# Optimization experiments

Hardware: AMD Instinct MI355X
Metric: run time of the kernel (lower is better)

The kernel has to match this reference:

```python
import jax, jax.numpy as jnp
import numpy as np

HID = 1024
NTOK = 16
BIAS_SCALE = 1.5
EPS = 1e-5


def layer_norm(x, g, b):
    mu = jnp.mean(x, axis=-1, keepdims=True)
    var = jnp.mean(jnp.square(x - mu), axis=-1, keepdims=True)
    return (x - mu) * jax.lax.rsqrt(var + EPS) * g + b


def setup_inputs() -> dict:
    key = jax.random.key(0)
    ks = jax.random.split(key, 16)
    B, T = 8, 4096
    Dt, Ds, Dp = 512, 512, 64
    Din = Dt + Ds + Dp

    def lin(k, fan_in, fan_out):
        bound = 1.0 / np.sqrt(fan_in)
        k1, k2 = jax.random.split(k)
        W = jax.random.uniform(k1, (fan_in, fan_out), jnp.float32, -bound, bound)
        b = jax.random.uniform(k2, (fan_out,), jnp.float32, -bound, bound)
        return W, b

    W_in, b_in = lin(ks[0], Din, HID)
    W_m1, b_m1 = lin(ks[1], HID, HID)
    W_m2, b_m2 = lin(ks[2], HID, HID)
    W_o1, b_o1 = lin(ks[3], HID, HID // 2)
    W_o2, b_o2 = lin(ks[4], HID // 2, 1)
    return {
        "trace_features": jax.random.normal(ks[5], (B, T, Dt), jnp.float32),
        "semantic_features": jax.random.normal(ks[6], (B, T, Ds), jnp.float32),
        "prior_features": jax.random.normal(ks[7], (B, T, Dp), jnp.float32),
        "W_in": W_in, "b_in": b_in,
        "ln_in_g": jnp.ones((HID,), jnp.float32), "ln_in_b": jnp.zeros((HID,), jnp.float32),
        "W_m1": W_m1, "b_m1": b_m1, "W_m2": W_m2, "b_m2": b_m2,
        "W_o1": W_o1, "b_o1": b_o1, "W_o2": W_o2, "b_o2": b_o2,
        "token_queries": jax.random.normal(ks[8], (NTOK, HID), jnp.float32) * 0.02,
        "ln_out_g": jnp.ones((HID,), jnp.float32), "ln_out_b": jnp.zeros((HID,), jnp.float32),
    }


def reference(trace_features, semantic_features, prior_features,
              W_in, b_in, ln_in_g, ln_in_b,
              W_m1, b_m1, W_m2, b_m2,
              W_o1, b_o1, W_o2, b_o2,
              token_queries, ln_out_g, ln_out_b):
    # fuse inputs: [B, T, Dt+Ds+Dp]
    fused = jnp.concatenate([trace_features, semantic_features, prior_features], axis=-1)
    h = fused @ W_in + b_in  # [B, T, H]
    mlp = jax.nn.gelu(h @ W_m1 + b_m1, approximate=False) @ W_m2 + b_m2
    seq_hidden = layer_norm(h + mlp, ln_in_g, ln_in_b)

    # objectness head -> [B, T]
    obj_logits = (jax.nn.gelu(seq_hidden @ W_o1 + b_o1, approximate=False) @ W_o2 + b_o2)[..., 0]
    objectness = jax.nn.sigmoid(obj_logits)

    # learned-query cross attention with objectness bias
    scale = float(HID) ** -0.5
    attn_logits = jnp.einsum('nh,bth->bnt', token_queries, seq_hidden) * scale
    attn_logits = attn_logits + BIAS_SCALE * objectness[:, None, :]
    attn = jax.nn.softmax(attn_logits, axis=-1)  # [B, N, T]
    token_values = jnp.einsum('bnt,bth->bnh', attn, seq_hidden)
    state_tokens = layer_norm(token_queries[None] + token_values, ln_out_g, ln_out_b)
    return state_tokens, attn, objectness
```

## Files before the change

### kernel.cpp

```cpp
#include <hip/hip_runtime.h>
#include <hip/hip_bf16.h>
#include <math.h>

typedef __bf16 bf16;
typedef __bf16 bf16x8 __attribute__((ext_vector_type(8)));
typedef __bf16 bf16x4 __attribute__((ext_vector_type(4)));
typedef float f32x4 __attribute__((ext_vector_type(4)));

#define KM 32768

__device__ __forceinline__ void gload16(const void* g, void* l) {
  __builtin_amdgcn_global_load_lds((const __attribute__((address_space(1))) void*)g,
                                   (__attribute__((address_space(3))) void*)l, 16, 0, 0);
}

__device__ __forceinline__ float gelu_exact(float x) {
  return 0.5f * x * (1.0f + erff(x * 0.70710678118654752f));
}

__global__ void fuse_kernel(const float* __restrict__ tr, const float* __restrict__ se,
                            const float* __restrict__ pr, bf16* __restrict__ Xb) {
  int g = blockIdx.x * 256 + threadIdx.x;
  if (g >= KM * 272) return;
  int m = g / 272;
  int k0 = (g - m * 272) * 4;
  float4 v;
  if (k0 < 512)       v = *reinterpret_cast<const float4*>(tr + (size_t)m * 512 + k0);
  else if (k0 < 1024) v = *reinterpret_cast<const float4*>(se + (size_t)m * 512 + (k0 - 512));
  else                v = *reinterpret_cast<const float4*>(pr + (size_t)m * 64 + (k0 - 1024));
  union { bf16 h[4]; ushort4 u; } p;
  p.h[0] = (bf16)v.x; p.h[1] = (bf16)v.y; p.h[2] = (bf16)v.z; p.h[3] = (bf16)v.w;
  *reinterpret_cast<ushort4*>(Xb + (size_t)m * 1088 + k0) = p.u;
}

__global__ void transpose_all(const float* __restrict__ W_in, const float* __restrict__ W_m1,
                              const float* __restrict__ W_m2, const float* __restrict__ W_o1,
                              bf16* __restrict__ WbIn, bf16* __restrict__ WbM1,
                              bf16* __restrict__ WbM2, bf16* __restrict__ WbO1) {
  __shared__ float t[32][33];
  int b = blockIdx.x;
  const float* W; bf16* Wt; int K, N, kb, nb;
  if (b < 1088)      { W = W_in; Wt = WbIn; K = 1088; N = 1024; kb = b % 34;  nb = b / 34; }
  else if (b < 2112) { int c = b - 1088; W = W_m1; Wt = WbM1; K = 1024; N = 1024; kb = c & 31; nb = c >> 5; }
  else if (b < 3136) { int c = b - 2112; W = W_m2; Wt = WbM2; K = 1024; N = 1024; kb = c & 31; nb = c >> 5; }
  else               { int c = b - 3136; W = W_o1; Wt = WbO1; K = 1024; N = 512;  kb = c & 31; nb = c >> 5; }
  int k0 = kb * 32, n0 = nb * 32;
  int tx = threadIdx.x & 31, ty = threadIdx.x >> 5;
  #pragma unroll
  for (int j = 0; j < 32; j += 8) t[ty + j][tx] = W[(size_t)(k0 + ty + j) * N + n0 + tx];
  __syncthreads();
  #pragma unroll
  for (int j = 0; j < 32; j += 8)
    Wt[(size_t)(n0 + ty + j) * K + k0 + tx] = (bf16)t[tx][ty + j];
}

template<int ACT, bool RES, bool OBJ>
__global__ void gemm_kernel(const bf16* __restrict__ A, const bf16* __restrict__ Bt,
                            const float* __restrict__ bias, const bf16* __restrict__ res,
                            bf16* __restrict__ C, const float* __restrict__ w2,
                            float* __restrict__ objp, int N, int K, int nbn) {
  __shared__ __align__(16) bf16 lds[2][128 * 64];
  int nwg = gridDim.x;
  int bid0 = blockIdx.x;
  int bid = (nwg & 7) ? bid0 : ((bid0 & 7) * (nwg >> 3) + (bid0 >> 3));
  int bn = bid % nbn, bm = bid / nbn;
  int tid = threadIdx.x;
  int w = tid >> 6, L = tid & 63;
  int wm = w >> 1, wn = w & 1;
  int srow = L >> 3;
  int scol = 8 * ((L & 7) ^ srow);
  const bf16* Ab = A + (size_t)(bm * 128) * K;
  const bf16* Bb = Bt + (size_t)(bn * 128) * K;
  f32x4 acc[4][4] = {};
  int nkt = (K + 63) >> 6;
  for (int kt = 0; kt < nkt; ++kt) {
    int k0 = kt << 6;
    #pragma unroll
    for (int i = 0; i < 4; ++i) {
      int row = w * 32 + i * 8;
      gload16(Ab + (size_t)(row + srow) * K + k0 + scol, &lds[0][row * 64]);
      gload16(Bb + (size_t)(row + srow) * K + k0 + scol, &lds[1][row * 64]);
    }
    __syncthreads();
    #pragma unroll
    for (int kk = 0; kk < 2; ++kk) {
      bf16x8 af[4], bfr[4];
      int cb = kk * 64 + ((L >> 4) * 16);
      #pragma unroll
      for (int m = 0; m < 4; ++m) {
        int r = wm * 64 + m * 16 + (L & 15);
        int addr = r * 128 + (cb ^ ((r & 7) << 4));
        af[m] = *reinterpret_cast<const bf16x8*>(
            reinterpret_cast<const char*>(&lds[0][0]) + addr);
      }
      #pragma unroll
      for (int n = 0; n < 4; ++n) {
        int r = wn * 64 + n * 16 + (L & 15);
        int addr = r * 128 + (cb ^ ((r & 7) << 4));
        bfr[n] = *reinterpret_cast<const bf16x8*>(
            reinterpret_cast<const char*>(&lds[1][0]) + addr);
      }
      #pragma unroll
      for (int m = 0; m < 4; ++m)
        #pragma unroll
        for (int n = 0; n < 4; ++n)
          acc[m][n] = __builtin_amdgcn_mfma_f32_16x16x32_bf16(af[m], bfr[n], acc[m][n], 0, 0, 0);
    }
    __syncthreads();
  }
  int cn0 = bn * 128 + wn * 64;
  float bv[4];
  #pragma unroll
  for (int n = 0; n < 4; ++n) bv[n] = bias[cn0 + n * 16 + (L & 15)];
  if (OBJ) {
    float w2v[4];
    #pragma unroll
    for (int n = 0; n < 4; ++n) w2v[n] = w2[cn0 + n * 16 + (L & 15)];
    float* op = objp + (size_t)(bn * 2 + wn) * KM;
    #pragma unroll
    for (int m = 0; m < 4; ++m) {
      int grow0 = bm * 128 + wm * 64 + m * 16 + ((L >> 4) << 2);
      #pragma unroll
      for (int r = 0; r < 4; ++r) {
        float s = 0.f;
        #pragma unroll
        for (int n = 0; n < 4; ++n) {
          float v = gelu_exact(acc[m][n][r] + bv[n]);
          s += v * w2v[n];
        }
        s += __shfl_xor(s, 1); s += __shfl_xor(s, 2);
        s += __shfl_xor(s, 4); s += __shfl_xor(s, 8);
        if ((L & 15) == 0) op[grow0 + r] = s;
      }
    }
  } else {
    #pragma unroll
    for (int m = 0; m < 4; ++m) {
      int grow0 = bm * 128 + wm * 64 + m * 16 + ((L >> 4) << 2);
      #pragma unroll
      for (int r = 0; r < 4; ++r) {
        size_t ro = (size_t)(grow0 + r) * N;
        #pragma unroll
        for (int n = 0; n < 4; ++n) {
          float v = acc[m][n][r] + bv[n];
          if (ACT == 1) v = gelu_exact(v);
          int col = cn0 + n * 16 + (L & 15);
          if (RES) v += (float)res[ro + col];
          C[ro + col] = (bf16)v;
        }
      }
    }
  }
}

__global__ void ln_wave_kernel(bf16* __restrict__ X, const float* __restrict__ g,
                               const float* __restrict__ b) {
  int w = threadIdx.x >> 6, L = threadIdx.x & 63;
  size_t row = (size_t)blockIdx.x * 4 + w;
  bf16* xr = X + row * 1024 + L * 16;
  bf16x8 v0 = *reinterpret_cast<const bf16x8*>(xr);
  bf16x8 v1 = *reinterpret_cast<const bf16x8*>(xr + 8);
  float x[16];
  #pragma unroll
  for (int i = 0; i < 8; ++i) { x[i] = (float)v0[i]; x[8 + i] = (float)v1[i]; }
  float s = 0.f;
  #pragma unroll
  for (int i = 0; i < 16; ++i) s += x[i];
  #pragma unroll
  for (int off = 32; off > 0; off >>= 1) s += __shfl_xor(s, off);
  float mu = s * (1.0f / 1024.0f);
  float sq = 0.f;
  #pragma unroll
  for (int i = 0; i < 16; ++i) { x[i] -= mu; sq += x[i] * x[i]; }
  #pragma unroll
  for (int off = 32; off > 0; off >>= 1) sq += __shfl_xor(sq, off);
  float rs = rsqrtf(sq * (1.0f / 1024.0f) + 1e-5f);
  const float4* gp = reinterpret_cast<const float4*>(g + L * 16);
  const float4* bp = reinterpret_cast<const float4*>(b + L * 16);
  bf16x8 o0, o1;
  #pragma unroll
  for (int q = 0; q < 4; ++q) {
    float4 gv = gp[q], bv = bp[q];
    int i = q * 4;
    float r0 = x[i] * rs * gv.x + bv.x;
    float r1 = x[i + 1] * rs * gv.y + bv.y;
    float r2 = x[i + 2] * rs * gv.z + bv.z;
    float r3 = x[i + 3] * rs * gv.w + bv.w;
    if (q < 2) { o0[i] = (bf16)r0; o0[i + 1] = (bf16)r1; o0[i + 2] = (bf16)r2; o0[i + 3] = (bf16)r3; }
    else { o1[i - 8] = (bf16)r0; o1[i - 7] = (bf16)r1; o1[i - 6] = (bf16)r2; o1[i - 5] = (bf16)r3; }
  }
  *reinterpret_cast<bf16x8*>(xr) = o0;
  *reinterpret_cast<bf16x8*>(xr + 8) = o1;
}

__global__ void attn_logits_mfma(const bf16* __restrict__ seq, const float* __restrict__ tq,
                                 const float* __restrict__ objp, const float* __restrict__ b2,
                                 float* __restrict__ logits, float* __restrict__ out_obj) {
  __shared__ bf16 tqs[16][1032];
  int tid = threadIdx.x;
  for (int i = tid; i < 4096; i += 256) {
    int idx = i * 4;
    int n = idx >> 10, k = idx & 1023;
    float4 v = *reinterpret_cast<const float4*>(tq + idx);
    bf16x4 p; p[0] = (bf16)v.x; p[1] = (bf16)v.y; p[2] = (bf16)v.z; p[3] = (bf16)v.w;
    *reinterpret_cast<bf16x4*>(&tqs[n][k]) = p;
  }
  __syncthreads();
  int w = tid >> 6, L = tid & 63;
  int row0 = blockIdx.x * 128 + w * 32;
  const bf16* A0 = seq + (size_t)(row0 + (L & 15)) * 1024 + ((L >> 4) * 8);
  const bf16* Bq = &tqs[L & 15][(L >> 4) * 8];
  f32x4 acc0 = {}, acc1 = {};
  #pragma unroll 4
  for (int kt = 0; kt < 32; ++kt) {
    int k0 = kt * 32;
    bf16x8 bq = *reinterpret_cast<const bf16x8*>(Bq + k0);
    bf16x8 a0 = *reinterpret_cast<const bf16x8*>(A0 + k0);
    bf16x8 a1 = *reinterpret_cast<const bf16x8*>(A0 + 16 * 1024 + k0);
    acc0 = __builtin_amdgcn_mfma_f32_16x16x32_bf16(a0, bq, acc0, 0, 0, 0);
    acc1 = __builtin_amdgcn_mfma_f32_16x16x32_bf16(a1, bq, acc1, 0, 0, 0);
  }
  float b2v = b2[0];
  int b = row0 >> 12;
  int n = L & 15;
  float* outn = logits + ((size_t)(b * 16) + n) * 4096;
  #pragma unroll
  for (int mf = 0; mf < 2; ++mf) {
    int mrow = row0 + mf * 16 + ((L >> 4) << 2);
    float os0 = 0.f, os1 = 0.f, os2 = 0.f, os3 = 0.f;
    #pragma unroll
    for (int p = 0; p < 8; ++p) {
      float4 t = *reinterpret_cast<const float4*>(objp + (size_t)p * KM + mrow);
      os0 += t.x; os1 += t.y; os2 += t.z; os3 += t.w;
    }
    float ob[4];
    ob[0] = 1.0f / (1.0f + expf(-(os0 + b2v)));
    ob[1] = 1.0f / (1.0f + expf(-(os1 + b2v)));
    ob[2] = 1.0f / (1.0f + expf(-(os2 + b2v)));
    ob[3] = 1.0f / (1.0f + expf(-(os3 + b2v)));
    #pragma unroll
    for (int r = 0; r < 4; ++r) {
      int m = mrow + r;
      float v = (mf == 0 ? acc0[r] : acc1[r]) * 0.03125f + 1.5f * ob[r];
      outn[m & 4095] = v;
    }
    if (n == 0) {
      float4 o4 = make_float4(ob[0], ob[1], ob[2], ob[3]);
      *reinterpret_cast<float4*>(out_obj + mrow) = o4;
    }
  }
}

__global__ void softmax_kernel(const float* __restrict__ logits, float* __restrict__ attn) {
  __shared__ float sb[4];
  size_t row = blockIdx.x;
  const float* lr = logits + row * 4096;
  float* orow = attn + row * 4096;
  int tid = threadIdx.x;
  float x[16];
  #pragma unroll
  for (int i = 0; i < 4; ++i) {
    float4 v = *reinterpret_cast<const float4*>(lr + tid * 16 + i * 4);
    x[i * 4 + 0] = v.x; x[i * 4 + 1] = v.y; x[i * 4 + 2] = v.z; x[i * 4 + 3] = v.w;
  }
  float mx = -1e30f;
  #pragma unroll
  for (int j = 0; j < 16; ++j) mx = fmaxf(mx, x[j]);
  #pragma unroll
  for (int off = 32; off > 0; off >>= 1) mx = fmaxf(mx, __shfl_xor(mx, off));
  if ((tid & 63) == 0) sb[tid >> 6] = mx;
  __syncthreads();
  mx = fmaxf(fmaxf(sb[0], sb[1]), fmaxf(sb[2], sb[3]));
  __syncthreads();
  float s = 0.f;
  #pragma unroll
  for (int j = 0; j < 16; ++j) { x[j] = expf(x[j] - mx); s += x[j]; }
  #pragma unroll
  for (int off = 32; off > 0; off >>= 1) s += __shfl_xor(s, off);
  if ((tid & 63) == 0) sb[tid >> 6] = s;
  __syncthreads();
  float inv = 1.0f / (sb[0] + sb[1] + sb[2] + sb[3]);
  #pragma unroll
  for (int i = 0; i < 4; ++i) {
    float4 v = make_float4(x[i * 4] * inv, x[i * 4 + 1] * inv, x[i * 4 + 2] * inv, x[i * 4 + 3] * inv);
    *reinterpret_cast<float4*>(orow + tid * 16 + i * 4) = v;
  }
}

__global__ void token_values_kernel(const float* __restrict__ attn, const bf16* __restrict__ seq,
                                    float* __restrict__ tvp) {
  int bid = blockIdx.x;
  int split = bid & 3;
  int hc = (bid >> 2) & 15;
  int b = bid >> 6;
  __shared__ float al[16][256];
  int h = hc * 64 + (threadIdx.x & 63);
  int grp = threadIdx.x >> 6;
  float acc[4] = {0.f, 0.f, 0.f, 0.f};
  for (int c = 0; c < 4; ++c) {
    int t0 = split * 1024 + c * 256;
    __syncthreads();
    for (int i = threadIdx.x; i < 4096; i += 256)
      al[i >> 8][i & 255] = attn[((size_t)b * 16 + (i >> 8)) * 4096 + t0 + (i & 255)];
    __syncthreads();
    for (int tt = 0; tt < 256; ++tt) {
      float s = (float)seq[((size_t)b * 4096 + t0 + tt) * 1024 + h];
      #pragma unroll
      for (int i = 0; i < 4; ++i) acc[i] += al[grp * 4 + i][tt] * s;
    }
  }
  #pragma unroll
  for (int i = 0; i < 4; ++i)
    tvp[(size_t)split * 131072 + ((size_t)b * 16 + grp * 4 + i) * 1024 + h] = acc[i];
}

__global__ void final_ln_kernel(const float* __restrict__ tq, const float* __restrict__ tvp,
                                const float* __restrict__ g, const float* __restrict__ bb,
                                float* __restrict__ out0) {
  __shared__ float sb[4];
  int row = blockIdx.x;
  int n = row & 15;
  int tid = threadIdx.x;
  float x[4];
  #pragma unroll
  for (int i = 0; i < 4; ++i) {
    int h = tid * 4 + i;
    float v = tq[n * 1024 + h];
    #pragma unroll
    for (int p = 0; p < 4; ++p) v += tvp[(size_t)p * 131072 + (size_t)row * 1024 + h];
    x[i] = v;
  }
  float s = x[0] + x[1] + x[2] + x[3];
  #pragma unroll
  for (int off = 32; off > 0; off >>= 1) s += __shfl_xor(s, off);
  if ((tid & 63) == 0) sb[tid >> 6] = s;
  __syncthreads();
  float mu = (sb[0] + sb[1] + sb[2] + sb[3]) * (1.0f / 1024.0f);
  __syncthreads();
  float d[4], sq = 0.f;
  #pragma unroll
  for (int i = 0; i < 4; ++i) { d[i] = x[i] - mu; sq += d[i] * d[i]; }
  #pragma unroll
  for (int off = 32; off > 0; off >>= 1) sq += __shfl_xor(sq, off);
  if ((tid & 63) == 0) sb[tid >> 6] = sq;
  __syncthreads();
  float var = (sb[0] + sb[1] + sb[2] + sb[3]) * (1.0f / 1024.0f);
  float rs = rsqrtf(var + 1e-5f);
  #pragma unroll
  for (int i = 0; i < 4; ++i) {
    int h = tid * 4 + i;
    out0[(size_t)row * 1024 + h] = d[i] * rs * g[h] + bb[h];
  }
}

extern "C" void kernel_launch(void* const* d_in, const int* in_sizes, int n_in,
                              void* d_out, int out_size, void* d_ws, size_t ws_size,
                              hipStream_t stream) {
  const float* tr      = (const float*)d_in[0];
  const float* se      = (const float*)d_in[1];
  const float* pr      = (const float*)d_in[2];
  const float* W_in    = (const float*)d_in[3];
  const float* b_in    = (const float*)d_in[4];
  const float* ln_in_g = (const float*)d_in[5];
  const float* ln_in_b = (const float*)d_in[6];
  const float* W_m1    = (const float*)d_in[7];
  const float* b_m1    = (const float*)d_in[8];
  const float* W_m2    = (const float*)d_in[9];
  const float* b_m2    = (const float*)d_in[10];
  const float* W_o1    = (const float*)d_in[11];
  const float* b_o1    = (const float*)d_in[12];
  const float* W_o2    = (const float*)d_in[13];
  const float* b_o2    = (const float*)d_in[14];
  const float* tq      = (const float*)d_in[15];
  const float* ln_out_g= (const float*)d_in[16];
  const float* ln_out_b= (const float*)d_in[17];

  float* out       = (float*)d_out;
  float* out_state = out;
  float* out_attn  = out + 131072;
  float* out_obj   = out + 131072 + 524288;

  char* ws = (char*)d_ws;
  size_t off = 0;
  auto alloc = [&](size_t bytes) {
    char* p = ws + off;
    off += (bytes + 255) & ~(size_t)255;
    return p;
  };
  bf16*  Xb   = (bf16*)alloc(71303168);
  bf16*  t1   = Xb;
  bf16*  hb   = (bf16*)alloc(67108864);
  bf16*  sq   = (bf16*)alloc(67108864);
  bf16*  WbIn = (bf16*)alloc(2228224);
  bf16*  WbM1 = (bf16*)alloc(2097152);
  bf16*  WbM2 = (bf16*)alloc(2097152);
  bf16*  WbO1 = (bf16*)alloc(1048576);
  float* objp = (float*)alloc(8 * KM * 4);
  float* logw = (float*)alloc(2097152);
  float* tvp  = (float*)alloc(2097152);

  fuse_kernel<<<(KM * 272 + 255) / 256, 256, 0, stream>>>(tr, se, pr, Xb);
  transpose_all<<<3648, 256, 0, stream>>>(W_in, W_m1, W_m2, W_o1, WbIn, WbM1, WbM2, WbO1);

  gemm_kernel<0, false, false><<<2048, 256, 0, stream>>>(
      Xb, WbIn, b_in, nullptr, hb, nullptr, nullptr, 1024, 1088, 8);
  gemm_kernel<1, false, false><<<2048, 256, 0, stream>>>(
      hb, WbM1, b_m1, nullptr, t1, nullptr, nullptr, 1024, 1024, 8);
  gemm_kernel<0, true, false><<<2048, 256, 0, stream>>>(
      t1, WbM2, b_m2, hb, sq, nullptr, nullptr, 1024, 1024, 8);
  ln_wave_kernel<<<8192, 256, 0, stream>>>(sq, ln_in_g, ln_in_b);
  gemm_kernel<1, false, true><<<1024, 256, 0, stream>>>(
      sq, WbO1, b_o1, nullptr, nullptr, W_o2, objp, 512, 1024, 4);
  attn_logits_mfma<<<256, 256, 0, stream>>>(sq, tq, objp, b_o2, logw, out_obj);
  softmax_kernel<<<128, 256, 0, stream>>>(logw, out_attn);
  token_values_kernel<<<512, 256, 0, stream>>>(out_attn, sq, tvp);
  final_ln_kernel<<<128, 256, 0, stream>>>(tq, tvp, ln_out_g, ln_out_b, out_state);
}
```

Baseline: 458.5 us.

## Use 32x32 MFMA in GEMMs, merge prep kernels, split token values wider

The GEMM inner loop switches from 16x16x32 to 32x32x16 bf16 MFMA tiles, with a 2x2 fragment layout per wave and a matching epilogue. This cuts the number of LDS fragment reads per MFMA flop. The input-fusion and weight-transpose kernels are merged into one launch, and softmax now runs in place on the output attention buffer, dropping a scratch buffer. Token values are split 16 ways over T instead of 4 to get more blocks, at the cost of more partial sums for the final LN to reduce.

```diff
diff --git a/kernel.cpp b/kernel.cpp
--- a/kernel.cpp
+++ b/kernel.cpp
@@ -5,7 +5,7 @@
 typedef __bf16 bf16;
 typedef __bf16 bf16x8 __attribute__((ext_vector_type(8)));
 typedef __bf16 bf16x4 __attribute__((ext_vector_type(4)));
-typedef float f32x4 __attribute__((ext_vector_type(4)));
+typedef float f32x16 __attribute__((ext_vector_type(16)));
 
 #define KM 32768
 
@@ -18,27 +18,28 @@
   return 0.5f * x * (1.0f + erff(x * 0.70710678118654752f));
 }
 
-__global__ void fuse_kernel(const float* __restrict__ tr, const float* __restrict__ se,
-                            const float* __restrict__ pr, bf16* __restrict__ Xb) {
-  int g = blockIdx.x * 256 + threadIdx.x;
-  if (g >= KM * 272) return;
-  int m = g / 272;
-  int k0 = (g - m * 272) * 4;
-  float4 v;
-  if (k0 < 512)       v = *reinterpret_cast<const float4*>(tr + (size_t)m * 512 + k0);
-  else if (k0 < 1024) v = *reinterpret_cast<const float4*>(se + (size_t)m * 512 + (k0 - 512));
-  else                v = *reinterpret_cast<const float4*>(pr + (size_t)m * 64 + (k0 - 1024));
-  union { bf16 h[4]; ushort4 u; } p;
-  p.h[0] = (bf16)v.x; p.h[1] = (bf16)v.y; p.h[2] = (bf16)v.z; p.h[3] = (bf16)v.w;
-  *reinterpret_cast<ushort4*>(Xb + (size_t)m * 1088 + k0) = p.u;
-}
-
-__global__ void transpose_all(const float* __restrict__ W_in, const float* __restrict__ W_m1,
-                              const float* __restrict__ W_m2, const float* __restrict__ W_o1,
-                              bf16* __restrict__ WbIn, bf16* __restrict__ WbM1,
-                              bf16* __restrict__ WbM2, bf16* __restrict__ WbO1) {
+__global__ void fuse_transpose_kernel(const float* __restrict__ tr, const float* __restrict__ se,
+                                      const float* __restrict__ pr, bf16* __restrict__ Xb,
+                                      const float* __restrict__ W_in, const float* __restrict__ W_m1,
+                                      const float* __restrict__ W_m2, const float* __restrict__ W_o1,
+                                      bf16* __restrict__ WbIn, bf16* __restrict__ WbM1,
+                                      bf16* __restrict__ WbM2, bf16* __restrict__ WbO1) {
+  int bid = blockIdx.x;
+  if (bid < 34816) {
+    int g = bid * 256 + threadIdx.x;
+    int m = g / 272;
+    int k0 = (g - m * 272) * 4;
+    float4 v;
+    if (k0 < 512)       v = *reinterpret_cast<const float4*>(tr + (size_t)m * 512 + k0);
+    else if (k0 < 1024) v = *reinterpret_cast<const float4*>(se + (size_t)m * 512 + (k0 - 512));
+    else                v = *reinterpret_cast<const float4*>(pr + (size_t)m * 64 + (k0 - 1024));
+    union { bf16 h[4]; ushort4 u; } p;
+    p.h[0] = (bf16)v.x; p.h[1] = (bf16)v.y; p.h[2] = (bf16)v.z; p.h[3] = (bf16)v.w;
+    *reinterpret_cast<ushort4*>(Xb + (size_t)m * 1088 + k0) = p.u;
+    return;
+  }
   __shared__ float t[32][33];
-  int b = blockIdx.x;
+  int b = bid - 34816;
   const float* W; bf16* Wt; int K, N, kb, nb;
   if (b < 1088)      { W = W_in; Wt = WbIn; K = 1088; N = 1024; kb = b % 34;  nb = b / 34; }
   else if (b < 2112) { int c = b - 1088; W = W_m1; Wt = WbM1; K = 1024; N = 1024; kb = c & 31; nb = c >> 5; }
@@ -71,7 +72,7 @@
   int scol = 8 * ((L & 7) ^ srow);
   const bf16* Ab = A + (size_t)(bm * 128) * K;
   const bf16* Bb = Bt + (size_t)(bn * 128) * K;
-  f32x4 acc[4][4] = {};
+  f32x16 acc[2][2] = {};
   int nkt = (K + 63) >> 6;
   for (int kt = 0; kt < nkt; ++kt) {
     int k0 = kt << 6;
@@ -83,71 +84,60 @@
     }
     __syncthreads();
     #pragma unroll
-    for (int kk = 0; kk < 2; ++kk) {
-      bf16x8 af[4], bfr[4];
-      int cb = kk * 64 + ((L >> 4) * 16);
+    for (int kk = 0; kk < 4; ++kk) {
+      bf16x8 af[2], bfr[2];
+      int cb = kk * 32 + ((L >> 5) * 16);
       #pragma unroll
-      for (int m = 0; m < 4; ++m) {
-        int r = wm * 64 + m * 16 + (L & 15);
-        int addr = r * 128 + (cb ^ ((r & 7) << 4));
-        af[m] = *reinterpret_cast<const bf16x8*>(
-            reinterpret_cast<const char*>(&lds[0][0]) + addr);
+      for (int mf = 0; mf < 2; ++mf) {
+        int r = wm * 64 + mf * 32 + (L & 31);
+        af[mf] = *reinterpret_cast<const bf16x8*>(
+            reinterpret_cast<const char*>(&lds[0][0]) + r * 128 + (cb ^ ((r & 7) << 4)));
       }
       #pragma unroll
-      for (int n = 0; n < 4; ++n) {
-        int r = wn * 64 + n * 16 + (L & 15);
-        int addr = r * 128 + (cb ^ ((r & 7) << 4));
-        bfr[n] = *reinterpret_cast<const bf16x8*>(
-            reinterpret_cast<const char*>(&lds[1][0]) + addr);
+      for (int nf = 0; nf < 2; ++nf) {
+        int r = wn * 64 + nf * 32 + (L & 31);
+        bfr[nf] = *reinterpret_cast<const bf16x8*>(
+            reinterpret_cast<const char*>(&lds[1][0]) + r * 128 + (cb ^ ((r & 7) << 4)));
       }
       #pragma unroll
-      for (int m = 0; m < 4; ++m)
+      for (int mf = 0; mf < 2; ++mf)
         #pragma unroll
-        for (int n = 0; n < 4; ++n)
-          acc[m][n] = __builtin_amdgcn_mfma_f32_16x16x32_bf16(af[m], bfr[n], acc[m][n], 0, 0, 0);
+        for (int nf = 0; nf < 2; ++nf)
+          acc[mf][nf] = __builtin_amdgcn_mfma_f32_32x32x16_bf16(af[mf], bfr[nf], acc[mf][nf], 0, 0, 0);
     }
     __syncthreads();
   }
-  int cn0 = bn * 128 + wn * 64;
-  float bv[4];
-  #pragma unroll
-  for (int n = 0; n < 4; ++n) bv[n] = bias[cn0 + n * 16 + (L & 15)];
+  int colv = bn * 128 + wn * 64 + (L & 31);
+  float bv0 = bias[colv], bv1 = bias[colv + 32];
   if (OBJ) {
-    float w2v[4];
-    #pragma unroll
-    for (int n = 0; n < 4; ++n) w2v[n] = w2[cn0 + n * 16 + (L & 15)];
+    float w20 = w2[colv], w21 = w2[colv + 32];
     float* op = objp + (size_t)(bn * 2 + wn) * KM;
     #pragma unroll
-    for (int m = 0; m < 4; ++m) {
-      int grow0 = bm * 128 + wm * 64 + m * 16 + ((L >> 4) << 2);
+    for (int mf = 0; mf < 2; ++mf) {
+      int rowbase = bm * 128 + wm * 64 + mf * 32 + ((L >> 5) << 2);
       #pragma unroll
-      for (int r = 0; r < 4; ++r) {
-        float s = 0.f;
-        #pragma unroll
-        for (int n = 0; n < 4; ++n) {
-          float v = gelu_exact(acc[m][n][r] + bv[n]);
-          s += v * w2v[n];
-        }
+      for (int reg = 0; reg < 16; ++reg) {
+        float s = gelu_exact(acc[mf][0][reg] + bv0) * w20 +
+                  gelu_exact(acc[mf][1][reg] + bv1) * w21;
         s += __shfl_xor(s, 1); s += __shfl_xor(s, 2);
-        s += __shfl_xor(s, 4); s += __shfl_xor(s, 8);
-        if ((L & 15) == 0) op[grow0 + r] = s;
+        s += __shfl_xor(s, 4); s += __shfl_xor(s, 8); s += __shfl_xor(s, 16);
+        if ((L & 31) == 0) op[rowbase + (reg & 3) + 8 * (reg >> 2)] = s;
       }
     }
   } else {
     #pragma unroll
-    for (int m = 0; m < 4; ++m) {
-      int grow0 = bm * 128 + wm * 64 + m * 16 + ((L >> 4) << 2);
+    for (int mf = 0; mf < 2; ++mf) {
+      int rowbase = bm * 128 + wm * 64 + mf * 32 + ((L >> 5) << 2);
       #pragma unroll
-      for (int r = 0; r < 4; ++r) {
-        size_t ro = (size_t)(grow0 + r) * N;
-        #pragma unroll
-        for (int n = 0; n < 4; ++n) {
-          float v = acc[m][n][r] + bv[n];
-          if (ACT == 1) v = gelu_exact(v);
-          int col = cn0 + n * 16 + (L & 15);
-          if (RES) v += (float)res[ro + col];
-          C[ro + col] = (bf16)v;
-        }
+      for (int reg = 0; reg < 16; ++reg) {
+        int rr = rowbase + (reg & 3) + 8 * (reg >> 2);
+        size_t ro = (size_t)rr * N;
+        float v0 = acc[mf][0][reg] + bv0;
+        float v1 = acc[mf][1][reg] + bv1;
+        if (ACT == 1) { v0 = gelu_exact(v0); v1 = gelu_exact(v1); }
+        if (RES) { v0 += (float)res[ro + colv]; v1 += (float)res[ro + colv + 32]; }
+        C[ro + colv] = (bf16)v0;
+        C[ro + colv + 32] = (bf16)v1;
       }
     }
   }
@@ -210,6 +200,7 @@
   int row0 = blockIdx.x * 128 + w * 32;
   const bf16* A0 = seq + (size_t)(row0 + (L & 15)) * 1024 + ((L >> 4) * 8);
   const bf16* Bq = &tqs[L & 15][(L >> 4) * 8];
+  typedef float f32x4 __attribute__((ext_vector_type(4)));
   f32x4 acc0 = {}, acc1 = {};
   #pragma unroll 4
   for (int kt = 0; kt < 32; ++kt) {
@@ -251,16 +242,15 @@
   }
 }
 
-__global__ void softmax_kernel(const float* __restrict__ logits, float* __restrict__ attn) {
+__global__ void softmax_kernel(float* __restrict__ attn) {
   __shared__ float sb[4];
   size_t row = blockIdx.x;
-  const float* lr = logits + row * 4096;
   float* orow = attn + row * 4096;
   int tid = threadIdx.x;
   float x[16];
   #pragma unroll
   for (int i = 0; i < 4; ++i) {
-    float4 v = *reinterpret_cast<const float4*>(lr + tid * 16 + i * 4);
+    float4 v = *reinterpret_cast<const float4*>(orow + tid * 16 + i * 4);
     x[i * 4 + 0] = v.x; x[i * 4 + 1] = v.y; x[i * 4 + 2] = v.z; x[i * 4 + 3] = v.w;
   }
   float mx = -1e30f;
@@ -290,24 +280,21 @@
 __global__ void token_values_kernel(const float* __restrict__ attn, const bf16* __restrict__ seq,
                                     float* __restrict__ tvp) {
   int bid = blockIdx.x;
-  int split = bid & 3;
-  int hc = (bid >> 2) & 15;
-  int b = bid >> 6;
+  int split = bid & 15;
+  int hc = (bid >> 4) & 15;
+  int b = bid >> 8;
   __shared__ float al[16][256];
   int h = hc * 64 + (threadIdx.x & 63);
   int grp = threadIdx.x >> 6;
+  int t0 = split * 256;
+  for (int i = threadIdx.x; i < 4096; i += 256)
+    al[i >> 8][i & 255] = attn[((size_t)b * 16 + (i >> 8)) * 4096 + t0 + (i & 255)];
+  __syncthreads();
   float acc[4] = {0.f, 0.f, 0.f, 0.f};
-  for (int c = 0; c < 4; ++c) {
-    int t0 = split * 1024 + c * 256;
-    __syncthreads();
-    for (int i = threadIdx.x; i < 4096; i += 256)
-      al[i >> 8][i & 255] = attn[((size_t)b * 16 + (i >> 8)) * 4096 + t0 + (i & 255)];
-    __syncthreads();
-    for (int tt = 0; tt < 256; ++tt) {
-      float s = (float)seq[((size_t)b * 4096 + t0 + tt) * 1024 + h];
-      #pragma unroll
-      for (int i = 0; i < 4; ++i) acc[i] += al[grp * 4 + i][tt] * s;
-    }
+  for (int tt = 0; tt < 256; ++tt) {
+    float s = (float)seq[((size_t)b * 4096 + t0 + tt) * 1024 + h];
+    #pragma unroll
+    for (int i = 0; i < 4; ++i) acc[i] += al[grp * 4 + i][tt] * s;
   }
   #pragma unroll
   for (int i = 0; i < 4; ++i)
@@ -327,7 +314,7 @@
     int h = tid * 4 + i;
     float v = tq[n * 1024 + h];
     #pragma unroll
-    for (int p = 0; p < 4; ++p) v += tvp[(size_t)p * 131072 + (size_t)row * 1024 + h];
+    for (int p = 0; p < 16; ++p) v += tvp[(size_t)p * 131072 + (size_t)row * 1024 + h];
     x[i] = v;
   }
   float s = x[0] + x[1] + x[2] + x[3];
@@ -396,11 +383,10 @@
   bf16*  WbM2 = (bf16*)alloc(2097152);
   bf16*  WbO1 = (bf16*)alloc(1048576);
   float* objp = (float*)alloc(8 * KM * 4);
-  float* logw = (float*)alloc(2097152);
-  float* tvp  = (float*)alloc(2097152);
-
-  fuse_kernel<<<(KM * 272 + 255) / 256, 256, 0, stream>>>(tr, se, pr, Xb);
-  transpose_all<<<3648, 256, 0, stream>>>(W_in, W_m1, W_m2, W_o1, WbIn, WbM1, WbM2, WbO1);
+  float* tvp  = (float*)alloc(16 * 131072 * 4);
+
+  fuse_transpose_kernel<<<34816 + 3648, 256, 0, stream>>>(
+      tr, se, pr, Xb, W_in, W_m1, W_m2, W_o1, WbIn, WbM1, WbM2, WbO1);
 
   gemm_kernel<0, false, false><<<2048, 256, 0, stream>>>(
       Xb, WbIn, b_in, nullptr, hb, nullptr, nullptr, 1024, 1088, 8);
@@ -411,8 +397,8 @@
   ln_wave_kernel<<<8192, 256, 0, stream>>>(sq, ln_in_g, ln_in_b);
   gemm_kernel<1, false, true><<<1024, 256, 0, stream>>>(
       sq, WbO1, b_o1, nullptr, nullptr, W_o2, objp, 512, 1024, 4);
-  attn_logits_mfma<<<256, 256, 0, stream>>>(sq, tq, objp, b_o2, logw, out_obj);
-  softmax_kernel<<<128, 256, 0, stream>>>(logw, out_attn);
-  token_values_kernel<<<512, 256, 0, stream>>>(out_attn, sq, tvp);
+  attn_logits_mfma<<<256, 256, 0, stream>>>(sq, tq, objp, b_o2, out_attn, out_obj);
+  softmax_kernel<<<128, 256, 0, stream>>>(out_attn);
+  token_values_kernel<<<2048, 256, 0, stream>>>(out_attn, sq, tvp);
   final_ln_kernel<<<128, 256, 0, stream>>>(tq, tvp, ln_out_g, ln_out_b, out_state);
 }
```

Measured after the change: 450.7 us. Within noise of the previous version (-1.7%).
